# Optimization experiments

Measured on AMD Instinct MI355X. Metric: run time of the kernel, lower is better.

## Reference

```python
import jax, jax.numpy as jnp
import numpy as np

B, S, E = 8, 1024, 1024
H, HS = 16, 64  # num_heads, head_size; H*HS == E


def setup_inputs() -> dict:
    key = jax.random.key(0)
    ks = jax.random.split(key, 6)
    scale = 1.0 / np.sqrt(E)
    x = jax.random.normal(ks[0], (B, S, E), dtype=jnp.float32)
    # per-head projection weights stacked: [H, E, HS] (Linear(n_embd, head_size, bias=False))
    Wq = jax.random.normal(ks[1], (H, E, HS), dtype=jnp.float32) * scale
    Wk = jax.random.normal(ks[2], (H, E, HS), dtype=jnp.float32) * scale
    Wv = jax.random.normal(ks[3], (H, E, HS), dtype=jnp.float32) * scale
    # output projection Linear(n_embd, n_embd): torch weight [out, in] plus bias
    Wproj = jax.random.normal(ks[4], (E, E), dtype=jnp.float32) * scale
    bproj = jax.random.normal(ks[5], (E,), dtype=jnp.float32) * scale
    return {"x": x, "Wq": Wq, "Wk": Wk, "Wv": Wv, "Wproj": Wproj, "bproj": bproj}


def reference(x, Wq, Wk, Wv, Wproj, bproj):
    # q,k,v: [B, H, S, HS]
    q = jnp.einsum('bse,hed->bhsd', x, Wq)
    k = jnp.einsum('bse,hed->bhsd', x, Wk)
    v = jnp.einsum('bse,hed->bhsd', x, Wv)
    scores = jnp.einsum('bhsd,bhtd->bhst', q, k) * (HS ** -0.5)  # [B,H,S,S]
    causal = jnp.tril(jnp.ones((S, S), dtype=bool))
    scores = jnp.where(causal, scores, jnp.finfo(scores.dtype).min)
    attn = jax.nn.softmax(scores, axis=-1)
    out = jnp.einsum('bhst,bhtd->bhsd', attn, v)         # [B,H,S,HS]
    out = out.transpose(0, 2, 1, 3).reshape(B, S, H * HS)  # concat heads -> [B,S,E]
    return out @ Wproj.T + bproj  # dropout p=0 is identity
```

## Files before the change

kernel.cpp:

```cpp
#include <hip/hip_runtime.h>
#include <stdint.h>

#define DEVI __device__ __forceinline__

typedef __attribute__((ext_vector_type(8))) short bf16x8;
typedef __attribute__((ext_vector_type(4))) float floatx4;
typedef __attribute__((ext_vector_type(16))) float floatx16;

constexpr int Bb = 8, Ss = 1024, Ee = 1024, Hh = 16, HSs = 64;
constexpr int Mq = Bb * Ss;
constexpr int Nqkv = 3 * Hh * HSs;
constexpr int Kd = Ee;

DEVI unsigned short f2bf(float x) {
  union { float f; uint32_t u; } v; v.f = x;
  uint32_t r = v.u + 0x7FFFu + ((v.u >> 16) & 1u);
  return (unsigned short)(r >> 16);
}

DEVI uint32_t pk2(float a, float b) {
  return (uint32_t)f2bf(a) | ((uint32_t)f2bf(b) << 16);
}

DEVI bf16x8 mkfrag(uint32_t a, uint32_t b, uint32_t c, uint32_t d) {
  union { uint32_t u[4]; bf16x8 v; } x;
  x.u[0] = a; x.u[1] = b; x.u[2] = c; x.u[3] = d;
  return x.v;
}

DEVI floatx4 mfma16(bf16x8 a, bf16x8 b, floatx4 c) {
  return __builtin_amdgcn_mfma_f32_16x16x32_bf16(a, b, c, 0, 0, 0);
}
DEVI floatx16 mfma32(bf16x8 a, bf16x8 b, floatx16 c) {
  return __builtin_amdgcn_mfma_f32_32x32x16_bf16(a, b, c, 0, 0, 0);
}

DEVI void gload_lds16(const void* g, void* l) {
  __builtin_amdgcn_global_load_lds(
      (const __attribute__((address_space(1))) uint32_t*)(uintptr_t)g,
      (__attribute__((address_space(3))) uint32_t*)(uint32_t)(uintptr_t)l,
      16, 0, 0);
}

__global__ void cvt_f32_bf16(const float* __restrict__ in, unsigned short* __restrict__ out, int n) {
  int i = (blockIdx.x * blockDim.x + threadIdx.x) * 4;
  if (i >= n) return;
  float4 v = *(const float4*)&in[i];
  ushort4 o;
  o.x = f2bf(v.x); o.y = f2bf(v.y); o.z = f2bf(v.z); o.w = f2bf(v.w);
  *(ushort4*)(void*)&out[i] = o;
}

__global__ void cvt_wqkv(const float* __restrict__ Wq, const float* __restrict__ Wk,
                         const float* __restrict__ Wv, unsigned short* __restrict__ out) {
  __shared__ float tile[64][65];
  const int k0 = blockIdx.x * 64;
  const int hh = blockIdx.y;
  const int qkv = hh >> 4, h = hh & 15;
  const float* W = (qkv == 0) ? Wq : ((qkv == 1) ? Wk : Wv);
  const float scale = (qkv == 0) ? (0.125f * 1.44269504f) : 1.0f;
  const float* src = W + (size_t)h * Ee * HSs;
  const int c = threadIdx.x & 63, r4 = threadIdx.x >> 6;
#pragma unroll
  for (int rr = 0; rr < 16; ++rr) {
    int row = rr * 4 + r4;
    tile[row][c] = src[(size_t)(k0 + row) * HSs + c] * scale;
  }
  __syncthreads();
  const int base_n = qkv * 1024 + h * 64;
#pragma unroll
  for (int rr = 0; rr < 16; ++rr) {
    int hs = rr * 4 + r4;
    out[(size_t)(base_n + hs) * Kd + k0 + c] = f2bf(tile[c][hs]);
  }
}

template <int EPI>
__global__ __launch_bounds__(256, 2) void gemm_bt(
    const unsigned short* __restrict__ A, const unsigned short* __restrict__ Bt,
    unsigned short* __restrict__ Qb, unsigned short* __restrict__ Kb,
    unsigned short* __restrict__ Vtb, float* __restrict__ Out,
    const float* __restrict__ bias, int Mdim, int Ndim, int Kdim) {
  __shared__ __align__(16) unsigned short As[2][128 * 64];
  __shared__ __align__(16) unsigned short Bs[2][128 * 64];
  const int tid = threadIdx.x;
  const int lane = tid & 63;
  const int wid = tid >> 6;
  const int wm = wid >> 1, wn = wid & 1;
  const int m0 = blockIdx.y * 128;
  const int n0 = blockIdx.x * 128;
  const int srow = lane >> 3;
  const int schunk = (lane & 7) ^ srow;
  const int NT = Kdim >> 6;

  floatx4 acc[4][4];
#pragma unroll
  for (int i = 0; i < 4; ++i)
#pragma unroll
    for (int j = 0; j < 4; ++j) acc[i][j] = (floatx4)0.f;

  auto stage = [&](int kt, int b) {
#pragma unroll
    for (int j = 0; j < 4; ++j) {
      const int g = wid * 4 + j;
      const int row = g * 8 + srow;
      gload_lds16(A + (size_t)(m0 + row) * Kdim + kt * 64 + schunk * 8, &As[b][g * 512]);
      gload_lds16(Bt + (size_t)(n0 + row) * Kdim + kt * 64 + schunk * 8, &Bs[b][g * 512]);
    }
  };

  stage(0, 0);
  __syncthreads();

  for (int kt = 0; kt < NT; ++kt) {
    const int cur = kt & 1;
    if (kt + 1 < NT) stage(kt + 1, cur ^ 1);
    const unsigned short* Ap = As[cur];
    const unsigned short* Bp = Bs[cur];
#pragma unroll
    for (int kk = 0; kk < 2; ++kk) {
      const int c = kk * 4 + (lane >> 4);
      bf16x8 af[4], bf[4];
#pragma unroll
      for (int i = 0; i < 4; ++i) {
        const int ra = wm * 64 + i * 16 + (lane & 15);
        af[i] = *(const bf16x8*)&Ap[ra * 64 + ((c ^ (ra & 7)) << 3)];
        const int rb = wn * 64 + i * 16 + (lane & 15);
        bf[i] = *(const bf16x8*)&Bp[rb * 64 + ((c ^ (rb & 7)) << 3)];
      }
#pragma unroll
      for (int i = 0; i < 4; ++i)
#pragma unroll
        for (int j = 0; j < 4; ++j) acc[i][j] = mfma16(af[i], bf[j], acc[i][j]);
    }
    __syncthreads();
  }

  const int mrow0 = m0 + wm * 64 + ((lane >> 4) << 2);
  const int ncol0 = n0 + wn * 64 + (lane & 15);
  if (EPI == 0) {
#pragma unroll
    for (int i = 0; i < 4; ++i) {
#pragma unroll
      for (int j = 0; j < 4; ++j) {
        const int n = ncol0 + j * 16;
        const int qkv = n >> 10;
        const int h = (n & 1023) >> 6;
        const int hs = n & 63;
#pragma unroll
        for (int r = 0; r < 4; ++r) {
          const int m = mrow0 + i * 16 + r;
          const int b = m >> 10, s = m & 1023;
          const unsigned short bv = f2bf(acc[i][j][r]);
          if (qkv == 0)
            Qb[(((size_t)b * Hh + h) * Ss + s) * HSs + hs] = bv;
          else if (qkv == 1)
            Kb[(((size_t)b * Hh + h) * Ss + s) * HSs + hs] = bv;
          else
            Vtb[(((size_t)b * Hh + h) * HSs + hs) * Ss + s] = bv;
        }
      }
    }
  } else {
#pragma unroll
    for (int j = 0; j < 4; ++j) {
      const int n = ncol0 + j * 16;
      const float bj = bias[n];
#pragma unroll
      for (int i = 0; i < 4; ++i) {
#pragma unroll
        for (int r = 0; r < 4; ++r) {
          const int m = mrow0 + i * 16 + r;
          Out[(size_t)m * Ndim + n] = acc[i][j][r] + bj;
        }
      }
    }
  }
}

__global__ __launch_bounds__(512, 4) void attn(
    const unsigned short* __restrict__ Qb, const unsigned short* __restrict__ Kb,
    const unsigned short* __restrict__ Vtb, unsigned short* __restrict__ Ob) {
  __shared__ __align__(16) unsigned short Ks[3][64 * 64];
  __shared__ __align__(16) unsigned short Vs[3][64 * 64];

  const int tid = threadIdx.x;
  const int lane = tid & 63;
  const int wid = tid >> 6;
  const int ln = lane & 31;
  const int hi = lane >> 5;
  const int bh = blockIdx.x & 127;
  const int qs = blockIdx.x >> 7;
  const int q0 = (3 - qs) * 256;
  const int bI = bh >> 4, hI = bh & 15;
  const unsigned short* Qp = Qb + (size_t)bh * Ss * HSs;
  const unsigned short* Kp = Kb + (size_t)bh * Ss * HSs;
  const unsigned short* Vp = Vtb + (size_t)bh * HSs * Ss;
  const int qw = q0 + wid * 32;
  const int q = qw + ln;

  bf16x8 qf[4];
#pragma unroll
  for (int kc = 0; kc < 4; ++kc)
    qf[kc] = *(const bf16x8*)&Qp[(size_t)q * 64 + kc * 16 + hi * 8];

  floatx16 oacc[2];
  oacc[0] = (floatx16)0.f;
  oacc[1] = (floatx16)0.f;
  float mrow = -3.0e38f, lrow = 0.f;

  const int srow = lane >> 3;
  const int schunk = (lane & 7) ^ srow;
  const int nt = (q0 >> 6) + 4;

  auto stageKV = [&](int t, int b) {
    const int row = wid * 8 + srow;
    gload_lds16(Kp + (size_t)(t * 64 + row) * 64 + schunk * 8, &Ks[b][wid * 512]);
    gload_lds16(Vp + (size_t)row * Ss + t * 64 + schunk * 8, &Vs[b][wid * 512]);
  };

  stageKV(0, 0);
  stageKV(1, 1);
  asm volatile("s_waitcnt vmcnt(2)" ::: "memory");
  __builtin_amdgcn_s_barrier();

  for (int t = 0; t < nt; ++t) {
    const int cur = t % 3;
    const bool pf = (t + 2 < nt);
    if (pf) stageKV(t + 2, (t + 2) % 3);
    const int t0 = t * 64;

    if (t0 <= qw + 31) {
      const unsigned short* Kc = Ks[cur];
      const unsigned short* Vc = Vs[cur];
      floatx16 sc[2];
#pragma unroll
      for (int tt = 0; tt < 2; ++tt) {
        floatx16 s = (floatx16)0.f;
        __builtin_amdgcn_s_setprio(1);
#pragma unroll
        for (int kc = 0; kc < 4; ++kc) {
          const int row = tt * 32 + ln;
          bf16x8 kf = *(const bf16x8*)&Kc[row * 64 + ((((kc << 1) | hi) ^ (ln & 7)) << 3)];
          s = mfma32(kf, qf[kc], s);
        }
        __builtin_amdgcn_s_setprio(0);
        sc[tt] = s;
      }
      if (t0 + 63 > qw) {
#pragma unroll
        for (int tt = 0; tt < 2; ++tt)
#pragma unroll
          for (int r = 0; r < 16; ++r) {
            const int tg = t0 + tt * 32 + (r & 3) + 8 * (r >> 2) + 4 * hi;
            if (tg > q) sc[tt][r] = -1e30f;
          }
      }
      float mx = sc[0][0];
#pragma unroll
      for (int tt = 0; tt < 2; ++tt)
#pragma unroll
        for (int r = 0; r < 16; ++r) mx = fmaxf(mx, sc[tt][r]);
      mx = fmaxf(mx, __shfl_xor(mx, 32));
      const float mnew = fmaxf(mrow, mx);
      const float scal = __builtin_amdgcn_exp2f(mrow - mnew);
      mrow = mnew;
      float ss = 0.f;
#pragma unroll
      for (int tt = 0; tt < 2; ++tt)
#pragma unroll
        for (int r = 0; r < 16; ++r) {
          const float p = __builtin_amdgcn_exp2f(sc[tt][r] - mnew);
          sc[tt][r] = p;
          ss += p;
        }
      ss += __shfl_xor(ss, 32);
      lrow = lrow * scal + ss;
#pragma unroll
      for (int dt = 0; dt < 2; ++dt)
#pragma unroll
        for (int r = 0; r < 16; ++r) oacc[dt][r] *= scal;

      bf16x8 pf_[4];
#pragma unroll
      for (int tt = 0; tt < 2; ++tt)
#pragma unroll
        for (int fb = 0; fb < 2; ++fb) {
          const int b = fb * 8;
          const uint32_t w0 = pk2(sc[tt][b + 0], sc[tt][b + 1]);
          const uint32_t w1 = pk2(sc[tt][b + 2], sc[tt][b + 3]);
          const uint32_t w2 = pk2(sc[tt][b + 4], sc[tt][b + 5]);
          const uint32_t w3 = pk2(sc[tt][b + 6], sc[tt][b + 7]);
          const uint32_t x0 = (uint32_t)__shfl_xor((int)w0, 32);
          const uint32_t x1 = (uint32_t)__shfl_xor((int)w1, 32);
          const uint32_t x2 = (uint32_t)__shfl_xor((int)w2, 32);
          const uint32_t x3 = (uint32_t)__shfl_xor((int)w3, 32);
          pf_[tt * 2 + fb] = mkfrag(hi ? x2 : w0, hi ? x3 : w1, hi ? w2 : x0, hi ? w3 : x1);
        }
#pragma unroll
      for (int dt = 0; dt < 2; ++dt) {
        const int row = dt * 32 + ln;
        __builtin_amdgcn_s_setprio(1);
#pragma unroll
        for (int kc = 0; kc < 4; ++kc) {
          bf16x8 vf = *(const bf16x8*)&Vc[row * 64 + ((((kc << 1) | hi) ^ (ln & 7)) << 3)];
          oacc[dt] = mfma32(vf, pf_[kc], oacc[dt]);
        }
        __builtin_amdgcn_s_setprio(0);
      }
    }

    if (pf) { asm volatile("s_waitcnt vmcnt(2)" ::: "memory"); }
    else    { asm volatile("s_waitcnt vmcnt(0)" ::: "memory"); }
    __builtin_amdgcn_s_barrier();
  }

  const float inv = 1.0f / lrow;
  unsigned short* Op = Ob + ((size_t)bI * Ss + q) * Ee + hI * 64;
#pragma unroll
  for (int dt = 0; dt < 2; ++dt)
#pragma unroll
    for (int g4 = 0; g4 < 4; ++g4) {
      ushort4 o;
      o.x = f2bf(oacc[dt][g4 * 4 + 0] * inv);
      o.y = f2bf(oacc[dt][g4 * 4 + 1] * inv);
      o.z = f2bf(oacc[dt][g4 * 4 + 2] * inv);
      o.w = f2bf(oacc[dt][g4 * 4 + 3] * inv);
      *(ushort4*)(void*)&Op[dt * 32 + g4 * 8 + hi * 4] = o;
    }
}

extern "C" void kernel_launch(void* const* d_in, const int* in_sizes, int n_in,
                              void* d_out, int out_size, void* d_ws, size_t ws_size,
                              hipStream_t stream) {
  const float* x = (const float*)d_in[0];
  const float* Wq = (const float*)d_in[1];
  const float* Wk = (const float*)d_in[2];
  const float* Wv = (const float*)d_in[3];
  const float* Wproj = (const float*)d_in[4];
  const float* bproj = (const float*)d_in[5];
  float* out = (float*)d_out;

  char* ws = (char*)d_ws;
  unsigned short* xb     = (unsigned short*)(ws);
  unsigned short* wqkvb  = (unsigned short*)(ws + (16u << 20));
  unsigned short* wprojb = (unsigned short*)(ws + (22u << 20));
  unsigned short* Qb     = (unsigned short*)(ws + (24u << 20));
  unsigned short* Kb     = (unsigned short*)(ws + (40u << 20));
  unsigned short* Vtb    = (unsigned short*)(ws + (56u << 20));
  unsigned short* Obuf   = (unsigned short*)(ws + (72u << 20));

  cvt_f32_bf16<<<8192, 256, 0, stream>>>(x, xb, Bb * Ss * Ee);
  cvt_wqkv<<<dim3(16, 48), 256, 0, stream>>>(Wq, Wk, Wv, wqkvb);
  cvt_f32_bf16<<<1024, 256, 0, stream>>>(Wproj, wprojb, Ee * Ee);
  gemm_bt<0><<<dim3(Nqkv / 128, Mq / 128), 256, 0, stream>>>(
      xb, wqkvb, Qb, Kb, Vtb, nullptr, nullptr, Mq, Nqkv, Kd);
  attn<<<512, 512, 0, stream>>>(Qb, Kb, Vtb, Obuf);
  gemm_bt<1><<<dim3(Ee / 128, Mq / 128), 256, 0, stream>>>(
      Obuf, wprojb, nullptr, nullptr, nullptr, out, bproj, Mq, Ee, Kd);
}
```

Before: 167.5 us.

## Single-buffer GEMM LDS, raise occupancy, and remap blocks for XCD locality

The GEMM kernel drops LDS double buffering in favour of one stage buffer per operand, halving shared memory so launch bounds can request four blocks per CU instead of two. Loads for a tile are now issued and then synchronised before compute, so the single-block prefetch overlap is gone and latency hiding relies on the extra resident blocks. Launch changes to a 1D grid, with block indices remapped so that blocks landing on the same XCD (round-robin of 8) cover contiguous tiles along M. This is meant to improve L2 reuse per XCD. The higher occupancy target may also limit registers per thread and cause spills.

```diff
diff --git a/kernel.cpp b/kernel.cpp
--- a/kernel.cpp
+++ b/kernel.cpp
@@ -76,19 +76,26 @@
 }
 
 template <int EPI>
-__global__ __launch_bounds__(256, 2) void gemm_bt(
+__global__ __launch_bounds__(256, 4) void gemm_bt(
     const unsigned short* __restrict__ A, const unsigned short* __restrict__ Bt,
     unsigned short* __restrict__ Qb, unsigned short* __restrict__ Kb,
     unsigned short* __restrict__ Vtb, float* __restrict__ Out,
     const float* __restrict__ bias, int Mdim, int Ndim, int Kdim) {
-  __shared__ __align__(16) unsigned short As[2][128 * 64];
-  __shared__ __align__(16) unsigned short Bs[2][128 * 64];
+  __shared__ __align__(16) unsigned short As[128 * 64];
+  __shared__ __align__(16) unsigned short Bs[128 * 64];
   const int tid = threadIdx.x;
   const int lane = tid & 63;
   const int wid = tid >> 6;
   const int wm = wid >> 1, wn = wid & 1;
-  const int m0 = blockIdx.y * 128;
-  const int n0 = blockIdx.x * 128;
+
+  const int Mblk = Mdim >> 7;
+  const int nwg = gridDim.x;
+  const int cpx = nwg >> 3;
+  const int lin = blockIdx.x;
+  const int g = (lin & 7) * cpx + (lin >> 3);
+  const int m0 = (g % Mblk) * 128;
+  const int n0 = (g / Mblk) * 128;
+
   const int srow = lane >> 3;
   const int schunk = (lane & 7) ^ srow;
   const int NT = Kdim >> 6;
@@ -99,24 +106,15 @@
 #pragma unroll
     for (int j = 0; j < 4; ++j) acc[i][j] = (floatx4)0.f;
 
-  auto stage = [&](int kt, int b) {
+  for (int kt = 0; kt < NT; ++kt) {
 #pragma unroll
     for (int j = 0; j < 4; ++j) {
-      const int g = wid * 4 + j;
-      const int row = g * 8 + srow;
-      gload_lds16(A + (size_t)(m0 + row) * Kdim + kt * 64 + schunk * 8, &As[b][g * 512]);
-      gload_lds16(Bt + (size_t)(n0 + row) * Kdim + kt * 64 + schunk * 8, &Bs[b][g * 512]);
-    }
-  };
-
-  stage(0, 0);
-  __syncthreads();
-
-  for (int kt = 0; kt < NT; ++kt) {
-    const int cur = kt & 1;
-    if (kt + 1 < NT) stage(kt + 1, cur ^ 1);
-    const unsigned short* Ap = As[cur];
-    const unsigned short* Bp = Bs[cur];
+      const int gg = wid * 4 + j;
+      const int row = gg * 8 + srow;
+      gload_lds16(A + (size_t)(m0 + row) * Kdim + kt * 64 + schunk * 8, &As[gg * 512]);
+      gload_lds16(Bt + (size_t)(n0 + row) * Kdim + kt * 64 + schunk * 8, &Bs[gg * 512]);
+    }
+    __syncthreads();
 #pragma unroll
     for (int kk = 0; kk < 2; ++kk) {
       const int c = kk * 4 + (lane >> 4);
@@ -124,9 +122,9 @@
 #pragma unroll
       for (int i = 0; i < 4; ++i) {
         const int ra = wm * 64 + i * 16 + (lane & 15);
-        af[i] = *(const bf16x8*)&Ap[ra * 64 + ((c ^ (ra & 7)) << 3)];
+        af[i] = *(const bf16x8*)&As[ra * 64 + ((c ^ (ra & 7)) << 3)];
         const int rb = wn * 64 + i * 16 + (lane & 15);
-        bf[i] = *(const bf16x8*)&Bp[rb * 64 + ((c ^ (rb & 7)) << 3)];
+        bf[i] = *(const bf16x8*)&Bs[rb * 64 + ((c ^ (rb & 7)) << 3)];
       }
 #pragma unroll
       for (int i = 0; i < 4; ++i)
@@ -353,9 +351,9 @@
   cvt_f32_bf16<<<8192, 256, 0, stream>>>(x, xb, Bb * Ss * Ee);
   cvt_wqkv<<<dim3(16, 48), 256, 0, stream>>>(Wq, Wk, Wv, wqkvb);
   cvt_f32_bf16<<<1024, 256, 0, stream>>>(Wproj, wprojb, Ee * Ee);
-  gemm_bt<0><<<dim3(Nqkv / 128, Mq / 128), 256, 0, stream>>>(
+  gemm_bt<0><<<(Nqkv / 128) * (Mq / 128), 256, 0, stream>>>(
       xb, wqkvb, Qb, Kb, Vtb, nullptr, nullptr, Mq, Nqkv, Kd);
   attn<<<512, 512, 0, stream>>>(Qb, Kb, Vtb, Obuf);
-  gemm_bt<1><<<dim3(Ee / 128, Mq / 128), 256, 0, stream>>>(
+  gemm_bt<1><<<(Ee / 128) * (Mq / 128), 256, 0, stream>>>(
       Obuf, wprojb, nullptr, nullptr, nullptr, out, bproj, Mq, Ee, Kd);
 }
```

New measurement: 184.0 us. 1.1x slower.

## Split GEMM into QKV kernel with BK=32 double buffer and single-buffered projection

Applied to the files above, without the earlier changes.

Splits the templated GEMM into two specialized kernels. The QKV GEMM now uses a K-tile of 32 with a double buffer, a new XOR swizzle and launch bounds of 4 blocks per CU, so it uses half the LDS per block and should raise occupancy. The projection GEMM drops double buffering to a single 64-wide LDS stage with a sync before compute, which also cuts LDS use but removes load/compute overlap. Having more K iterations adds synchronization overhead and may put pressure on register allocation under the tighter launch bound.

```diff
diff --git a/kernel.cpp b/kernel.cpp
--- a/kernel.cpp
+++ b/kernel.cpp
@@ -75,23 +75,20 @@
   }
 }
 
-template <int EPI>
-__global__ __launch_bounds__(256, 2) void gemm_bt(
+__global__ __launch_bounds__(256, 4) void gemm_qkv_db32(
     const unsigned short* __restrict__ A, const unsigned short* __restrict__ Bt,
     unsigned short* __restrict__ Qb, unsigned short* __restrict__ Kb,
-    unsigned short* __restrict__ Vtb, float* __restrict__ Out,
-    const float* __restrict__ bias, int Mdim, int Ndim, int Kdim) {
-  __shared__ __align__(16) unsigned short As[2][128 * 64];
-  __shared__ __align__(16) unsigned short Bs[2][128 * 64];
+    unsigned short* __restrict__ Vtb, int Kdim) {
+  __shared__ __align__(16) unsigned short As[2][128 * 32];
+  __shared__ __align__(16) unsigned short Bs[2][128 * 32];
   const int tid = threadIdx.x;
   const int lane = tid & 63;
   const int wid = tid >> 6;
   const int wm = wid >> 1, wn = wid & 1;
   const int m0 = blockIdx.y * 128;
   const int n0 = blockIdx.x * 128;
-  const int srow = lane >> 3;
-  const int schunk = (lane & 7) ^ srow;
-  const int NT = Kdim >> 6;
+  const int srow = lane >> 2;
+  const int NT = Kdim >> 5;
 
   floatx4 acc[4][4];
 #pragma unroll
@@ -101,22 +98,95 @@
 
   auto stage = [&](int kt, int b) {
 #pragma unroll
-    for (int j = 0; j < 4; ++j) {
-      const int g = wid * 4 + j;
-      const int row = g * 8 + srow;
-      gload_lds16(A + (size_t)(m0 + row) * Kdim + kt * 64 + schunk * 8, &As[b][g * 512]);
-      gload_lds16(Bt + (size_t)(n0 + row) * Kdim + kt * 64 + schunk * 8, &Bs[b][g * 512]);
+    for (int i = 0; i < 2; ++i) {
+      const int g = wid * 2 + i;
+      const int row = g * 16 + srow;
+      const int sch = (lane & 3) ^ ((row + (row >> 2)) & 3);
+      gload_lds16(A + (size_t)(m0 + row) * Kdim + kt * 32 + sch * 8, &As[b][g * 512]);
+      gload_lds16(Bt + (size_t)(n0 + row) * Kdim + kt * 32 + sch * 8, &Bs[b][g * 512]);
     }
   };
 
   stage(0, 0);
   __syncthreads();
 
+  const int c = lane >> 4;
   for (int kt = 0; kt < NT; ++kt) {
     const int cur = kt & 1;
     if (kt + 1 < NT) stage(kt + 1, cur ^ 1);
     const unsigned short* Ap = As[cur];
     const unsigned short* Bp = Bs[cur];
+    bf16x8 af[4], bf[4];
+#pragma unroll
+    for (int i = 0; i < 4; ++i) {
+      const int ra = wm * 64 + i * 16 + (lane & 15);
+      af[i] = *(const bf16x8*)&Ap[ra * 32 + ((c ^ ((ra + (ra >> 2)) & 3)) << 3)];
+      const int rb = wn * 64 + i * 16 + (lane & 15);
+      bf[i] = *(const bf16x8*)&Bp[rb * 32 + ((c ^ ((rb + (rb >> 2)) & 3)) << 3)];
+    }
+#pragma unroll
+    for (int i = 0; i < 4; ++i)
+#pragma unroll
+      for (int j = 0; j < 4; ++j) acc[i][j] = mfma16(af[i], bf[j], acc[i][j]);
+    __syncthreads();
+  }
+
+  const int mrow0 = m0 + wm * 64 + ((lane >> 4) << 2);
+  const int ncol0 = n0 + wn * 64 + (lane & 15);
+#pragma unroll
+  for (int i = 0; i < 4; ++i) {
+#pragma unroll
+    for (int j = 0; j < 4; ++j) {
+      const int n = ncol0 + j * 16;
+      const int qkv = n >> 10;
+      const int h = (n & 1023) >> 6;
+      const int hs = n & 63;
+#pragma unroll
+      for (int r = 0; r < 4; ++r) {
+        const int m = mrow0 + i * 16 + r;
+        const int b = m >> 10, s = m & 1023;
+        const unsigned short bv = f2bf(acc[i][j][r]);
+        if (qkv == 0)
+          Qb[(((size_t)b * Hh + h) * Ss + s) * HSs + hs] = bv;
+        else if (qkv == 1)
+          Kb[(((size_t)b * Hh + h) * Ss + s) * HSs + hs] = bv;
+        else
+          Vtb[(((size_t)b * Hh + h) * HSs + hs) * Ss + s] = bv;
+      }
+    }
+  }
+}
+
+__global__ __launch_bounds__(256, 2) void gemm_proj(
+    const unsigned short* __restrict__ A, const unsigned short* __restrict__ Bt,
+    float* __restrict__ Out, const float* __restrict__ bias, int Ndim, int Kdim) {
+  __shared__ __align__(16) unsigned short As[128 * 64];
+  __shared__ __align__(16) unsigned short Bs[128 * 64];
+  const int tid = threadIdx.x;
+  const int lane = tid & 63;
+  const int wid = tid >> 6;
+  const int wm = wid >> 1, wn = wid & 1;
+  const int m0 = blockIdx.y * 128;
+  const int n0 = blockIdx.x * 128;
+
+  floatx4 acc[4][4];
+#pragma unroll
+  for (int i = 0; i < 4; ++i)
+#pragma unroll
+    for (int j = 0; j < 4; ++j) acc[i][j] = (floatx4)0.f;
+
+  const int srow = lane >> 3;
+  const int schunk = (lane & 7) ^ srow;
+
+  for (int kt = 0; kt < Kdim; kt += 64) {
+#pragma unroll
+    for (int j = 0; j < 4; ++j) {
+      const int g = wid * 4 + j;
+      const int row = g * 8 + srow;
+      gload_lds16(A + (size_t)(m0 + row) * Kdim + kt + schunk * 8, &As[g * 8 * 64]);
+      gload_lds16(Bt + (size_t)(n0 + row) * Kdim + kt + schunk * 8, &Bs[g * 8 * 64]);
+    }
+    __syncthreads();
 #pragma unroll
     for (int kk = 0; kk < 2; ++kk) {
       const int c = kk * 4 + (lane >> 4);
@@ -124,9 +194,9 @@
 #pragma unroll
       for (int i = 0; i < 4; ++i) {
         const int ra = wm * 64 + i * 16 + (lane & 15);
-        af[i] = *(const bf16x8*)&Ap[ra * 64 + ((c ^ (ra & 7)) << 3)];
+        af[i] = *(const bf16x8*)&As[ra * 64 + ((c ^ (ra & 7)) << 3)];
         const int rb = wn * 64 + i * 16 + (lane & 15);
-        bf[i] = *(const bf16x8*)&Bp[rb * 64 + ((c ^ (rb & 7)) << 3)];
+        bf[i] = *(const bf16x8*)&Bs[rb * 64 + ((c ^ (rb & 7)) << 3)];
       }
 #pragma unroll
       for (int i = 0; i < 4; ++i)
@@ -138,41 +208,16 @@
 
   const int mrow0 = m0 + wm * 64 + ((lane >> 4) << 2);
   const int ncol0 = n0 + wn * 64 + (lane & 15);
-  if (EPI == 0) {
+#pragma unroll
+  for (int j = 0; j < 4; ++j) {
+    const int n = ncol0 + j * 16;
+    const float bj = bias[n];
 #pragma unroll
     for (int i = 0; i < 4; ++i) {
 #pragma unroll
-      for (int j = 0; j < 4; ++j) {
-        const int n = ncol0 + j * 16;
-        const int qkv = n >> 10;
-        const int h = (n & 1023) >> 6;
-        const int hs = n & 63;
-#pragma unroll
-        for (int r = 0; r < 4; ++r) {
-          const int m = mrow0 + i * 16 + r;
-          const int b = m >> 10, s = m & 1023;
-          const unsigned short bv = f2bf(acc[i][j][r]);
-          if (qkv == 0)
-            Qb[(((size_t)b * Hh + h) * Ss + s) * HSs + hs] = bv;
-          else if (qkv == 1)
-            Kb[(((size_t)b * Hh + h) * Ss + s) * HSs + hs] = bv;
-          else
-            Vtb[(((size_t)b * Hh + h) * HSs + hs) * Ss + s] = bv;
-        }
-      }
-    }
-  } else {
-#pragma unroll
-    for (int j = 0; j < 4; ++j) {
-      const int n = ncol0 + j * 16;
-      const float bj = bias[n];
-#pragma unroll
-      for (int i = 0; i < 4; ++i) {
-#pragma unroll
-        for (int r = 0; r < 4; ++r) {
-          const int m = mrow0 + i * 16 + r;
-          Out[(size_t)m * Ndim + n] = acc[i][j][r] + bj;
-        }
+      for (int r = 0; r < 4; ++r) {
+        const int m = mrow0 + i * 16 + r;
+        Out[(size_t)m * Ndim + n] = acc[i][j][r] + bj;
       }
     }
   }
@@ -353,9 +398,9 @@
   cvt_f32_bf16<<<8192, 256, 0, stream>>>(x, xb, Bb * Ss * Ee);
   cvt_wqkv<<<dim3(16, 48), 256, 0, stream>>>(Wq, Wk, Wv, wqkvb);
   cvt_f32_bf16<<<1024, 256, 0, stream>>>(Wproj, wprojb, Ee * Ee);
-  gemm_bt<0><<<dim3(Nqkv / 128, Mq / 128), 256, 0, stream>>>(
-      xb, wqkvb, Qb, Kb, Vtb, nullptr, nullptr, Mq, Nqkv, Kd);
+  gemm_qkv_db32<<<dim3(Nqkv / 128, Mq / 128), 256, 0, stream>>>(
+      xb, wqkvb, Qb, Kb, Vtb, Kd);
   attn<<<512, 512, 0, stream>>>(Qb, Kb, Vtb, Obuf);
-  gemm_bt<1><<<dim3(Ee / 128, Mq / 128), 256, 0, stream>>>(
-      Obuf, wprojb, nullptr, nullptr, nullptr, out, bproj, Mq, Ee, Kd);
-}
+  gemm_proj<<<dim3(Ee / 128, Mq / 128), 256, 0, stream>>>(
+      Obuf, wprojb, out, bproj, Ee, Kd);
+}
```

New measurement: 170.2 us. About the same (+1.6%).
